# Kernel optimization log

Measured on AMD Instinct MI355X. Metric: run time of the kernel, lower is better.

Reference implementation:

```python
import jax, jax.numpy as jnp
import numpy as np

D = 64
N_NODES = 100000
N_EDGES = 1600000
N_GRAPHS = 64
IN_CH = 128
EDGE_DIM = 7
N_CONVS = 3  # layers after conv_first


def seg_softmax(logits, seg, n):
    m = jax.ops.segment_max(logits, seg, num_segments=n)
    e = jnp.exp(logits - m[seg])
    s = jax.ops.segment_sum(e, seg, num_segments=n)
    return e / (s[seg] + 1e-16)


def tconv(h, src, dst, edge_attr, Wq, bq, Wk, bk, Wv, bv, We, Ws, bs):
    # PyG TransformerConv, heads=1, concat=True, root_weight=True
    q = h @ Wq + bq          # [N, D]
    k = h @ Wk + bk
    v = h @ Wv + bv
    e = edge_attr @ We       # [E, D] (lin_edge has no bias)
    ke = k[src] + e          # key + edge per message
    alpha = jnp.sum(q[dst] * ke, axis=-1) / jnp.sqrt(jnp.float32(D))
    a = seg_softmax(alpha, dst, N_NODES)               # softmax over in-neighbors
    msg = a[:, None] * (v[src] + e)                    # [E, D]
    out = jax.ops.segment_sum(msg, dst, num_segments=N_NODES)
    return out + h @ Ws + bs                           # skip (lin_skip)


def setup_inputs() -> dict:
    key = jax.random.key(0)
    ks = iter(jax.random.split(key, 64))
    nrm = lambda shp, s=0.05: jax.random.normal(next(ks), shp, dtype=jnp.float32) * s
    inp = {}
    inp['x'] = jax.random.normal(next(ks), (N_NODES, IN_CH), dtype=jnp.float32)
    inp['edge_index'] = jax.random.randint(next(ks), (2, N_EDGES), 0, N_NODES, dtype=jnp.int32)
    inp['edge_attr'] = jax.random.normal(next(ks), (N_EDGES, EDGE_DIM), dtype=jnp.float32)
    inp['batch'] = jnp.sort(jax.random.randint(next(ks), (N_NODES,), 0, N_GRAPHS, dtype=jnp.int32))
    inp['y'] = jax.random.normal(next(ks), (N_GRAPHS, 6), dtype=jnp.float32)
    # conv_first (IN_CH -> D)
    inp['Wq0'] = nrm((IN_CH, D)); inp['bq0'] = jnp.zeros((D,), jnp.float32)
    inp['Wk0'] = nrm((IN_CH, D)); inp['bk0'] = jnp.zeros((D,), jnp.float32)
    inp['Wv0'] = nrm((IN_CH, D)); inp['bv0'] = jnp.zeros((D,), jnp.float32)
    inp['We0'] = nrm((EDGE_DIM, D))
    inp['Ws0'] = nrm((IN_CH, D)); inp['bs0'] = jnp.zeros((D,), jnp.float32)
    # stacked conv layers (D -> D), leading axis = layer
    inp['Wq'] = nrm((N_CONVS, D, D)); inp['bq'] = jnp.zeros((N_CONVS, D), jnp.float32)
    inp['Wk'] = nrm((N_CONVS, D, D)); inp['bk'] = jnp.zeros((N_CONVS, D), jnp.float32)
    inp['Wv'] = nrm((N_CONVS, D, D)); inp['bv'] = jnp.zeros((N_CONVS, D), jnp.float32)
    inp['We'] = nrm((N_CONVS, EDGE_DIM, D))
    inp['Ws'] = nrm((N_CONVS, D, D)); inp['bs'] = jnp.zeros((N_CONVS, D), jnp.float32)
    # gate_nn: Linear(D,D)+ReLU+Linear(D,1)
    inp['g1W'] = nrm((D, D)); inp['g1b'] = jnp.zeros((D,), jnp.float32)
    inp['g2W'] = nrm((D, 1)); inp['g2b'] = jnp.zeros((1,), jnp.float32)
    # 6 MLPs, each 64->32->16->8->1, stacked on leading expert axis
    inp['m0W'] = nrm((6, D, 32)); inp['m0b'] = jnp.zeros((6, 32), jnp.float32)
    inp['m1W'] = nrm((6, 32, 16)); inp['m1b'] = jnp.zeros((6, 16), jnp.float32)
    inp['m2W'] = nrm((6, 16, 8)); inp['m2b'] = jnp.zeros((6, 8), jnp.float32)
    inp['m3W'] = nrm((6, 8, 1)); inp['m3b'] = jnp.zeros((6, 1), jnp.float32)
    return inp


def reference(x, edge_attr, y, Wq0, bq0, Wk0, bk0, Wv0, bv0, We0, Ws0, bs0,
              Wq, bq, Wk, bk, Wv, bv, We, Ws, bs,
              g1W, g1b, g2W, g2b,
              m0W, m0b, m1W, m1b, m2W, m2b, m3W, m3b,
              edge_index, batch):
    src, dst = edge_index[0], edge_index[1]
    elu = jax.nn.elu
    outs = []
    h = elu(tconv(x, src, dst, edge_attr, Wq0, bq0, Wk0, bk0, Wv0, bv0, We0, Ws0, bs0))
    outs.append(h)
    for i in range(N_CONVS):
        h = tconv(h, src, dst, edge_attr, Wq[i], bq[i], Wk[i], bk[i],
                  Wv[i], bv[i], We[i], Ws[i], bs[i])
        if i != N_CONVS - 1:
            h = elu(h)
        outs.append(h)
    # JumpingKnowledge 'max'
    h = jnp.max(jnp.stack(outs, axis=0), axis=0)          # [N, D]
    # Global soft attention pooling
    gate = jax.nn.relu(h @ g1W + g1b) @ g2W + g2b         # [N, 1]
    gate = seg_softmax(gate[:, 0], batch, N_GRAPHS)[:, None]
    pooled = jax.ops.segment_sum(gate * h, batch, num_segments=N_GRAPHS)  # [G, D]
    # 6-way MLP ensemble (elu hidden)
    a = elu(jnp.einsum('gd,edh->egh', pooled, m0W) + m0b[:, None, :])
    a = elu(jnp.einsum('egh,ehk->egk', a, m1W) + m1b[:, None, :])
    a = elu(jnp.einsum('egk,ekj->egj', a, m2W) + m2b[:, None, :])
    preds = jnp.einsum('egj,ejo->ego', a, m3W) + m3b[:, None, :]  # [6, G, 1]
    preds = preds[:, :, 0].T                               # [G, 6]
    losses = jnp.sqrt(jnp.mean((preds - y) ** 2, axis=0))  # RMSE per target
    total_loss = jnp.sum(losses)
    return preds, total_loss
```

## Files before the change

### kernel.cpp

```cpp
#include <hip/hip_runtime.h>
#include <math.h>

#define N_NODES 100000
#define N_EDGES 1600000
#define N_GRAPHS 64
#define IN_CH 128
#define DIM 64
#define N_CONVS 3
#define NBLK 196
#define NPASS 8
#define PASS_SZ 12500

typedef const float* fp;
typedef unsigned int u32;
typedef unsigned short u16;
typedef __attribute__((ext_vector_type(8))) short short8v;
typedef __attribute__((ext_vector_type(4))) float f32x4;

__device__ inline u16 rne_bf16(float f) {
    u32 u = __float_as_uint(f);
    return (u16)((u + 0x7fffu + ((u >> 16) & 1u)) >> 16);
}
__device__ inline float bf16lo_f(u32 w) { return __uint_as_float(w << 16); }
__device__ inline float bf16hi_f(u32 w) { return __uint_as_float(w & 0xffff0000u); }

__global__ __launch_bounds__(256) void count_kernel(const int* __restrict__ dst, int* __restrict__ cnt) {
    int j = blockIdx.x * 256 + threadIdx.x;
    if (j < N_EDGES) {
        int d = dst[j];
        if ((unsigned)d < N_NODES) atomicAdd(&cnt[d], 1);
    }
}

__global__ __launch_bounds__(512) void scan1_kernel(const int* __restrict__ cnt, int* __restrict__ rp,
                                                    int* __restrict__ blksum) {
    __shared__ int tmp[512];
    int t = threadIdx.x, i = blockIdx.x * 512 + t;
    int v0 = (i < N_NODES) ? cnt[i] : 0;
    tmp[t] = v0;
    __syncthreads();
    for (int off = 1; off < 512; off <<= 1) {
        int add = (t >= off) ? tmp[t - off] : 0;
        __syncthreads();
        tmp[t] += add;
        __syncthreads();
    }
    if (i < N_NODES) rp[i] = tmp[t] - v0;
    if (t == 511) blksum[blockIdx.x] = tmp[511];
}

__global__ __launch_bounds__(256) void scan2_kernel(int* __restrict__ blksum) {
    __shared__ int tmp[256];
    int t = threadIdx.x;
    int v0 = (t < NBLK) ? blksum[t] : 0;
    tmp[t] = v0;
    __syncthreads();
    for (int off = 1; off < 256; off <<= 1) {
        int add = (t >= off) ? tmp[t - off] : 0;
        __syncthreads();
        tmp[t] += add;
        __syncthreads();
    }
    if (t < NBLK) blksum[t] = tmp[t] - v0;
}

__global__ __launch_bounds__(512) void scan3_kernel(int* __restrict__ rp, const int* __restrict__ blksum,
                                                    int* __restrict__ cursor) {
    int t = threadIdx.x, i = blockIdx.x * 512 + t;
    if (i < N_NODES) {
        int v = rp[i] + blksum[blockIdx.x];
        rp[i] = v;
        cursor[i] = v;
    }
    if (i == 0) rp[N_NODES] = N_EDGES;
}

__global__ __launch_bounds__(256) void cvt_ea_kernel(fp ea, uint4* __restrict__ eab_orig) {
    int j = blockIdx.x * 256 + threadIdx.x;
    if (j < N_EDGES) {
        size_t sb = (size_t)j * 7;
        u16 b[8];
#pragma unroll
        for (int c = 0; c < 7; ++c) b[c] = rne_bf16(ea[sb + c]);
        b[7] = 0;
        uint4 o;
        o.x = b[0] | ((u32)b[1] << 16);
        o.y = b[2] | ((u32)b[3] << 16);
        o.z = b[4] | ((u32)b[5] << 16);
        o.w = b[6] | ((u32)b[7] << 16);
        eab_orig[j] = o;
    }
}

__global__ __launch_bounds__(256) void scatter_pass_kernel(const int* __restrict__ src,
                                                           const int* __restrict__ dst,
                                                           const uint4* __restrict__ eab_orig,
                                                           int* __restrict__ cursor,
                                                           int* __restrict__ csr_src,
                                                           uint4* __restrict__ eab, int lo, int hi) {
    int j = blockIdx.x * 256 + threadIdx.x;
    if (j < N_EDGES) {
        int d = dst[j];
        if (d < lo || d >= hi || (unsigned)d >= N_NODES) return;
        int pos = atomicAdd(&cursor[d], 1);
        if ((unsigned)pos < N_EDGES) {
            int s = src[j];
            csr_src[pos] = ((unsigned)s < N_NODES) ? s : 0;
            eab[pos] = eab_orig[j];
        }
    }
}

__global__ __launch_bounds__(256) void cvt_bf16_kernel(const float* __restrict__ in, u16* __restrict__ out,
                                                       int n4) {
    int i = blockIdx.x * 256 + threadIdx.x;
    if (i < n4) {
        float4 v = reinterpret_cast<const float4*>(in)[i];
        ushort4 o;
        o.x = rne_bf16(v.x); o.y = rne_bf16(v.y); o.z = rne_bf16(v.z); o.w = rne_bf16(v.w);
        reinterpret_cast<ushort4*>(out)[i] = o;
    }
}

__global__ __launch_bounds__(256) void packW_kernel(fp Wq, fp Wk, fp Wv, fp Ws, u16* __restrict__ Bp,
                                                    int K) {
    int total = (K / 32) * 16 * 512;
    int tid = blockIdx.x * 256 + threadIdx.x;
    if (tid >= total) return;
    int j = tid & 7, l = (tid >> 3) & 63, fragid = tid >> 9;
    int tk = fragid >> 4, gtn = fragid & 15;
    int k = tk * 32 + ((l >> 4) << 3) + j;
    int n = (gtn << 4) + (l & 15);
    int mat = n >> 6, cn = n & 63;
    fp W = mat == 0 ? Wq : mat == 1 ? Wk : mat == 2 ? Wv : Ws;
    Bp[tid] = rne_bf16(W[k * 64 + cn]);
}

template <int K>
__global__ __launch_bounds__(256) void gemm_mfma_kernel(
    const u16* __restrict__ A, const u16* __restrict__ Bp,
    fp bq, fp bk, fp bv, fp bs,
    float* __restrict__ q, u16* __restrict__ kvp16, float* __restrict__ skb) {
    constexpr int NTK = K / 32;
    int wave = threadIdx.x >> 6;
    int l = threadIdx.x & 63;
    int lr = l & 15, lg = l >> 4;
    int row0 = blockIdx.x * 32;
    short8v a[2][NTK];
#pragma unroll
    for (int mi = 0; mi < 2; ++mi)
#pragma unroll
        for (int tk = 0; tk < NTK; ++tk)
            a[mi][tk] = *reinterpret_cast<const short8v*>(
                &A[(size_t)(row0 + mi * 16 + lr) * K + tk * 32 + lg * 8]);
    f32x4 c[2][4] = {};
#pragma unroll
    for (int tn = 0; tn < 4; ++tn) {
        int gtn = wave * 4 + tn;
#pragma unroll
        for (int tk = 0; tk < NTK; ++tk) {
            short8v b = *reinterpret_cast<const short8v*>(&Bp[((size_t)(tk * 16 + gtn) * 64 + l) * 8]);
            c[0][tn] = __builtin_amdgcn_mfma_f32_16x16x32_bf16(a[0][tk], b, c[0][tn], 0, 0, 0);
            c[1][tn] = __builtin_amdgcn_mfma_f32_16x16x32_bf16(a[1][tk], b, c[1][tn], 0, 0, 0);
        }
    }
    fp bias = wave == 0 ? bq : wave == 1 ? bk : wave == 2 ? bv : bs;
#pragma unroll
    for (int tn = 0; tn < 4; ++tn) {
        int cl = tn * 16 + lr;
        float bb = bias[cl];
#pragma unroll
        for (int mi = 0; mi < 2; ++mi)
#pragma unroll
            for (int r = 0; r < 4; ++r) {
                size_t row = row0 + mi * 16 + lg * 4 + r;
                float val = c[mi][tn][r] + bb;
                if (wave == 0) q[row * 64 + cl] = val * 0.125f;
                else if (wave == 3) skb[row * 64 + cl] = val;
                else if (wave == 1) kvp16[(row * 64 + cl) * 2] = rne_bf16(val);
                else kvp16[(row * 64 + cl) * 2 + 1] = rne_bf16(val);
            }
    }
}

__global__ __launch_bounds__(256) void node_kernel(
    const float* __restrict__ qs, const u32* __restrict__ kvp,
    const float* __restrict__ skb, const uint4* __restrict__ eab, fp We,
    const int* __restrict__ row_ptr, const int* __restrict__ csr_src,
    u16* __restrict__ hb, float* __restrict__ hmax, int act, int initmax) {
    int tid = threadIdx.x;
    int lane = tid & 63;
    int g = lane >> 4, fl = lane & 15;
    int gbase = g << 4;
    int n = blockIdx.x * 16 + (tid >> 6) * 4 + g;
    int f0 = fl * 4;
    float4 q4 = *reinterpret_cast<const float4*>(&qs[(size_t)n * 64 + f0]);
    float qw[7];
#pragma unroll
    for (int c = 0; c < 7; ++c) {
        float4 w4 = *reinterpret_cast<const float4*>(&We[c * 64 + f0]);
        float t = q4.x * w4.x + q4.y * w4.y + q4.z * w4.z + q4.w * w4.w;
        t += __shfl_xor(t, 1);
        t += __shfl_xor(t, 2);
        t += __shfl_xor(t, 4);
        t += __shfl_xor(t, 8);
        qw[c] = t;
    }
    int beg = row_ptr[n], end = row_ptr[n + 1];
    float s = 0.f;
    float ax = 0.f, ay = 0.f, az = 0.f, aw = 0.f;
    float r[7];
#pragma unroll
    for (int c = 0; c < 7; ++c) r[c] = 0.f;

    for (int p = beg; p < end; p += 4) {
        int svi = p + (fl & 3);
        svi = svi < end ? svi : end - 1;
        int sv = csr_src[svi];
#pragma unroll
        for (int j = 0; j < 4; ++j) {
            int pj = p + j;
            int pc = pj < end ? pj : end - 1;
            int sn = __shfl(sv, gbase + j);
            uint4 kv4 = *reinterpret_cast<const uint4*>(&kvp[(size_t)sn * 64 + f0]);
            uint4 e4 = eab[pc];
            float e0 = bf16lo_f(e4.x), e1 = bf16hi_f(e4.x);
            float e2 = bf16lo_f(e4.y), e3 = bf16hi_f(e4.y);
            float e4f = bf16lo_f(e4.z), e5 = bf16hi_f(e4.z);
            float e6 = bf16lo_f(e4.w);
            float al = qw[0] * e0 + qw[1] * e1 + qw[2] * e2 + qw[3] * e3 +
                       qw[4] * e4f + qw[5] * e5 + qw[6] * e6;
            float kf0 = bf16lo_f(kv4.x), vf0 = bf16hi_f(kv4.x);
            float kf1 = bf16lo_f(kv4.y), vf1 = bf16hi_f(kv4.y);
            float kf2 = bf16lo_f(kv4.z), vf2 = bf16hi_f(kv4.z);
            float kf3 = bf16lo_f(kv4.w), vf3 = bf16hi_f(kv4.w);
            float d = q4.x * kf0 + q4.y * kf1 + q4.z * kf2 + q4.w * kf3;
            d += __shfl_xor(d, 1);
            d += __shfl_xor(d, 2);
            d += __shfl_xor(d, 4);
            d += __shfl_xor(d, 8);
            float pe = (pj < end) ? __expf(al + d) : 0.f;
            s += pe;
            ax += pe * vf0; ay += pe * vf1; az += pe * vf2; aw += pe * vf3;
            r[0] += pe * e0; r[1] += pe * e1; r[2] += pe * e2; r[3] += pe * e3;
            r[4] += pe * e4f; r[5] += pe * e5; r[6] += pe * e6;
        }
    }
    float inv = 1.f / (s + 1e-16f);
    float o0 = ax, o1 = ay, o2 = az, o3 = aw;
#pragma unroll
    for (int c = 0; c < 7; ++c) {
        o0 += We[c * 64 + f0 + 0] * r[c];
        o1 += We[c * 64 + f0 + 1] * r[c];
        o2 += We[c * 64 + f0 + 2] * r[c];
        o3 += We[c * 64 + f0 + 3] * r[c];
    }
    float4 sk4 = *reinterpret_cast<const float4*>(&skb[(size_t)n * 64 + f0]);
    float4 res;
    res.x = o0 * inv + sk4.x;
    res.y = o1 * inv + sk4.y;
    res.z = o2 * inv + sk4.z;
    res.w = o3 * inv + sk4.w;
    if (act) {
        res.x = res.x > 0.f ? res.x : (__expf(res.x) - 1.f);
        res.y = res.y > 0.f ? res.y : (__expf(res.y) - 1.f);
        res.z = res.z > 0.f ? res.z : (__expf(res.z) - 1.f);
        res.w = res.w > 0.f ? res.w : (__expf(res.w) - 1.f);
    }
    ushort4 hb4;
    hb4.x = rne_bf16(res.x); hb4.y = rne_bf16(res.y); hb4.z = rne_bf16(res.z); hb4.w = rne_bf16(res.w);
    *reinterpret_cast<ushort4*>(&hb[(size_t)n * 64 + f0]) = hb4;
    if (initmax) {
        *reinterpret_cast<float4*>(&hmax[(size_t)n * 64 + f0]) = res;
    } else {
        float4 hm = *reinterpret_cast<const float4*>(&hmax[(size_t)n * 64 + f0]);
        hm.x = fmaxf(hm.x, res.x);
        hm.y = fmaxf(hm.y, res.y);
        hm.z = fmaxf(hm.z, res.z);
        hm.w = fmaxf(hm.w, res.w);
        *reinterpret_cast<float4*>(&hmax[(size_t)n * 64 + f0]) = hm;
    }
}

__global__ __launch_bounds__(256) void gate_kernel(const float* __restrict__ h, fp g1W, fp g1b, fp g2W,
                                                   fp g2b, float* __restrict__ gate) {
    __shared__ float hs[4][64];
    int w = threadIdx.x >> 6, lane = threadIdx.x & 63;
    int n = blockIdx.x * 4 + w;
    hs[w][lane] = h[(size_t)n * 64 + lane];
    __syncthreads();
    float a = 0.f;
    for (int f = 0; f < 64; ++f) a += hs[w][f] * g1W[f * 64 + lane];
    a = fmaxf(a + g1b[lane], 0.f);
    float val = a * g2W[lane];
#pragma unroll
    for (int off = 32; off; off >>= 1) val += __shfl_xor(val, off);
    if (lane == 0) gate[n] = val + g2b[0];
}

__global__ __launch_bounds__(256) void starts_kernel(const int* __restrict__ batch, int* __restrict__ starts) {
    int i = blockIdx.x * 256 + threadIdx.x;
    if (i >= N_NODES) return;
    if (i == 0) {
        int b = batch[0];
        for (int g = 0; g <= b && g <= N_GRAPHS; ++g) starts[g] = 0;
    } else {
        int b0 = batch[i - 1], b1 = batch[i];
        for (int g = b0 + 1; g <= b1 && g <= N_GRAPHS; ++g) starts[g] = i;
    }
    if (i == N_NODES - 1) {
        int b = batch[i];
        for (int g = b + 1; g <= N_GRAPHS; ++g) starts[g] = N_NODES;
    }
}

__global__ __launch_bounds__(256) void pool_kernel(const float* __restrict__ h, const float* __restrict__ gate,
                                                   const int* __restrict__ starts, float* __restrict__ pooled) {
    int g = blockIdx.x;
    int beg = starts[g], end = starts[g + 1];
    int tid = threadIdx.x, lane = tid & 63, w = tid >> 6;
    __shared__ float red[4];
    __shared__ float accs[4][64];
    float m = -INFINITY;
    for (int i = beg + tid; i < end; i += 256) m = fmaxf(m, gate[i]);
#pragma unroll
    for (int off = 32; off; off >>= 1) m = fmaxf(m, __shfl_xor(m, off));
    if (lane == 0) red[w] = m;
    __syncthreads();
    m = fmaxf(fmaxf(red[0], red[1]), fmaxf(red[2], red[3]));
    __syncthreads();
    float s = 0.f;
    for (int i = beg + tid; i < end; i += 256) s += __expf(gate[i] - m);
#pragma unroll
    for (int off = 32; off; off >>= 1) s += __shfl_xor(s, off);
    if (lane == 0) red[w] = s;
    __syncthreads();
    s = red[0] + red[1] + red[2] + red[3] + 1e-16f;
    float acc = 0.f;
    for (int i = beg + w; i < end; i += 4) {
        float p = __expf(gate[i] - m);
        acc += p * h[(size_t)i * 64 + lane];
    }
    accs[w][lane] = acc;
    __syncthreads();
    if (w == 0) pooled[g * 64 + lane] = (accs[0][lane] + accs[1][lane] + accs[2][lane] + accs[3][lane]) / s;
}

__global__ __launch_bounds__(256) void mlp_kernel(const float* __restrict__ pooled, fp m0W, fp m0b, fp m1W,
                                                  fp m1b, fp m2W, fp m2b, fp m3W, fp m3b,
                                                  float* __restrict__ out) {
    int e = blockIdx.x, tid = threadIdx.x;
    __shared__ float P[64 * 64];
    __shared__ float A1[64 * 32];
    __shared__ float A2[64 * 16];
    __shared__ float A3[64 * 8];
    for (int i = tid; i < 64 * 64; i += 256) P[i] = pooled[i];
    __syncthreads();
    fp W0 = m0W + e * 64 * 32; fp B0 = m0b + e * 32;
    for (int i = tid; i < 64 * 32; i += 256) {
        int g = i >> 5, c = i & 31;
        float a = B0[c];
        for (int f = 0; f < 64; ++f) a += P[g * 64 + f] * W0[f * 32 + c];
        A1[i] = a > 0.f ? a : (__expf(a) - 1.f);
    }
    __syncthreads();
    fp W1 = m1W + e * 32 * 16; fp B1 = m1b + e * 16;
    for (int i = tid; i < 64 * 16; i += 256) {
        int g = i >> 4, c = i & 15;
        float a = B1[c];
        for (int f = 0; f < 32; ++f) a += A1[g * 32 + f] * W1[f * 16 + c];
        A2[i] = a > 0.f ? a : (__expf(a) - 1.f);
    }
    __syncthreads();
    fp W2 = m2W + e * 16 * 8; fp B2 = m2b + e * 8;
    for (int i = tid; i < 64 * 8; i += 256) {
        int g = i >> 3, c = i & 7;
        float a = B2[c];
        for (int f = 0; f < 16; ++f) a += A2[g * 16 + f] * W2[f * 8 + c];
        A3[i] = a > 0.f ? a : (__expf(a) - 1.f);
    }
    __syncthreads();
    fp W3 = m3W + e * 8;
    if (tid < 64) {
        int g = tid;
        float a = m3b[e];
        for (int j = 0; j < 8; ++j) a += A3[g * 8 + j] * W3[j];
        out[g * 6 + e] = a;
    }
}

__global__ __launch_bounds__(64) void loss_kernel(const float* __restrict__ preds, fp y,
                                                  float* __restrict__ out) {
    int lane = threadIdx.x;
    float lsum = 0.f;
    if (lane < 6) {
        float acc = 0.f;
        for (int g = 0; g < 64; ++g) {
            float d = preds[g * 6 + lane] - y[g * 6 + lane];
            acc += d * d;
        }
        lsum = sqrtf(acc / 64.f);
    }
#pragma unroll
    for (int off = 32; off; off >>= 1) lsum += __shfl_xor(lsum, off);
    if (lane == 0) out[384] = lsum;
}

extern "C" void kernel_launch(void* const* d_in, const int* in_sizes, int n_in, void* d_out, int out_size,
                              void* d_ws, size_t ws_size, hipStream_t stream) {
    bool dictOrder = (in_sizes[1] == 2 * N_EDGES);
    int iEI = dictOrder ? 1 : 33;
    int iEA = dictOrder ? 2 : 1;
    int iBT = dictOrder ? 3 : 34;
    int iY  = dictOrder ? 4 : 2;
    int w0  = dictOrder ? 5 : 3;

    fp x = (fp)d_in[0];
    const int* ei = (const int*)d_in[iEI];
    fp eattr = (fp)d_in[iEA];
    const int* batch = (const int*)d_in[iBT];
    fp y = (fp)d_in[iY];
    fp Wq0 = (fp)d_in[w0 + 0], bq0 = (fp)d_in[w0 + 1], Wk0 = (fp)d_in[w0 + 2], bk0 = (fp)d_in[w0 + 3];
    fp Wv0 = (fp)d_in[w0 + 4], bv0 = (fp)d_in[w0 + 5], We0 = (fp)d_in[w0 + 6];
    fp Ws0 = (fp)d_in[w0 + 7], bs0 = (fp)d_in[w0 + 8];
    fp Wq = (fp)d_in[w0 + 9], bq = (fp)d_in[w0 + 10], Wk = (fp)d_in[w0 + 11], bk = (fp)d_in[w0 + 12];
    fp Wv = (fp)d_in[w0 + 13], bv = (fp)d_in[w0 + 14], Wel = (fp)d_in[w0 + 15];
    fp Ws = (fp)d_in[w0 + 16], bs = (fp)d_in[w0 + 17];
    fp g1W = (fp)d_in[w0 + 18], g1b = (fp)d_in[w0 + 19], g2W = (fp)d_in[w0 + 20], g2b = (fp)d_in[w0 + 21];
    fp m0W = (fp)d_in[w0 + 22], m0b = (fp)d_in[w0 + 23], m1W = (fp)d_in[w0 + 24], m1b = (fp)d_in[w0 + 25];
    fp m2W = (fp)d_in[w0 + 26], m2b = (fp)d_in[w0 + 27], m3W = (fp)d_in[w0 + 28], m3b = (fp)d_in[w0 + 29];

    const int* srcArr = ei;
    const int* dstArr = ei + N_EDGES;

    char* wsp = (char*)d_ws;
    auto alloc = [&](size_t bytes) -> void* {
        void* p = (void*)wsp;
        wsp += (bytes + 255) & ~(size_t)255;
        return p;
    };
    float* q = (float*)alloc((size_t)N_NODES * 64 * 4);
    u32* kvp = (u32*)alloc((size_t)N_NODES * 64 * 4);
    float* skb = (float*)alloc((size_t)N_NODES * 64 * 4);
    u16* hb = (u16*)alloc((size_t)N_NODES * 64 * 2);
    u16* xb = (u16*)alloc((size_t)N_NODES * IN_CH * 2);
    float* hmax = (float*)alloc((size_t)N_NODES * 64 * 4);
    float* gate = (float*)alloc((size_t)N_NODES * 4);
    float* pooled = (float*)alloc(64 * 64 * 4);
    int* row_ptr = (int*)alloc((N_NODES + 1) * 4);
    int* cursor = (int*)alloc((size_t)N_NODES * 4);
    int* csr_src = (int*)alloc((size_t)N_EDGES * 4);
    uint4* eab = (uint4*)alloc((size_t)N_EDGES * 16);
    uint4* eab_orig = (uint4*)alloc((size_t)N_EDGES * 16);
    u16* Bp0 = (u16*)alloc((size_t)(IN_CH / 32) * 16 * 512 * 2);
    u16* Bp1 = (u16*)alloc((size_t)(DIM / 32) * 16 * 512 * 2);
    u16* Bp2 = (u16*)alloc((size_t)(DIM / 32) * 16 * 512 * 2);
    u16* Bp3 = (u16*)alloc((size_t)(DIM / 32) * 16 * 512 * 2);
    int* blksum = (int*)alloc(256 * 4);
    int* starts = (int*)alloc((N_GRAPHS + 1) * 4);
    (void)ws_size;
    (void)n_in;

    float* outF = (float*)d_out;

    hipMemsetAsync(cursor, 0, (size_t)N_NODES * 4, stream);
    count_kernel<<<(N_EDGES + 255) / 256, 256, 0, stream>>>(dstArr, cursor);
    scan1_kernel<<<NBLK, 512, 0, stream>>>(cursor, row_ptr, blksum);
    scan2_kernel<<<1, 256, 0, stream>>>(blksum);
    scan3_kernel<<<NBLK, 512, 0, stream>>>(row_ptr, blksum, cursor);
    cvt_ea_kernel<<<(N_EDGES + 255) / 256, 256, 0, stream>>>(eattr, eab_orig);
    for (int p = 0; p < NPASS; ++p)
        scatter_pass_kernel<<<(N_EDGES + 255) / 256, 256, 0, stream>>>(
            srcArr, dstArr, eab_orig, cursor, csr_src, eab, p * PASS_SZ, (p + 1) * PASS_SZ);
    cvt_bf16_kernel<<<(N_NODES * IN_CH / 4 + 255) / 256, 256, 0, stream>>>(x, xb, N_NODES * IN_CH / 4);
    packW_kernel<<<((IN_CH / 32) * 16 * 512 + 255) / 256, 256, 0, stream>>>(Wq0, Wk0, Wv0, Ws0, Bp0, IN_CH);
    u16* Bps[3] = {Bp1, Bp2, Bp3};
    for (int i = 0; i < N_CONVS; ++i)
        packW_kernel<<<((DIM / 32) * 16 * 512 + 255) / 256, 256, 0, stream>>>(
            Wq + i * 4096, Wk + i * 4096, Wv + i * 4096, Ws + i * 4096, Bps[i], DIM);

    int nodeGrid = N_NODES / 16;
    gemm_mfma_kernel<IN_CH><<<N_NODES / 32, 256, 0, stream>>>(xb, Bp0, bq0, bk0, bv0, bs0, q, (u16*)kvp, skb);
    node_kernel<<<nodeGrid, 256, 0, stream>>>(q, kvp, skb, eab, We0, row_ptr, csr_src, hb, hmax, 1, 1);
    for (int i = 0; i < N_CONVS; ++i) {
        gemm_mfma_kernel<DIM><<<N_NODES / 32, 256, 0, stream>>>(hb, Bps[i], bq + i * 64, bk + i * 64,
                                                                bv + i * 64, bs + i * 64, q, (u16*)kvp, skb);
        node_kernel<<<nodeGrid, 256, 0, stream>>>(q, kvp, skb, eab, Wel + i * 448, row_ptr,
                                                  csr_src, hb, hmax, (i < N_CONVS - 1) ? 1 : 0, 0);
    }
    gate_kernel<<<N_NODES / 4, 256, 0, stream>>>(hmax, g1W, g1b, g2W, g2b, gate);
    starts_kernel<<<(N_NODES + 255) / 256, 256, 0, stream>>>(batch, starts);
    pool_kernel<<<N_GRAPHS, 256, 0, stream>>>(hmax, gate, starts, pooled);
    mlp_kernel<<<6, 256, 0, stream>>>(pooled, m0W, m0b, m1W, m1b, m2W, m2b, m3W, m3b, outF);
    loss_kernel<<<1, 64, 0, stream>>>(outF, y, outF);
}
```

Baseline: 898.2 us.

## Parallelize attention pooling across nodes with atomics instead of per-graph blocks

Replaces the 64-block per-graph pooling kernel (which serially scanned ~1560 nodes per graph) with node-parallel kernels. The gate kernel now computes the per-graph max through an order-preserving uint encoding and atomicMax. A separate kernel computes the exponentials and per-graph sums with wave-level reductions. A chunked accumulation kernel then atomically adds gate-weighted features into pooled, and normalization moves into the MLP kernel. The aim is to remove the low-occupancy tail of pool_kernel, at the cost of three extra memsets, float atomics with nondeterministic ordering, and an extra pass over the gate array.

```diff
diff --git a/kernel.cpp b/kernel.cpp
--- a/kernel.cpp
+++ b/kernel.cpp
@@ -23,6 +23,14 @@
 }
 __device__ inline float bf16lo_f(u32 w) { return __uint_as_float(w << 16); }
 __device__ inline float bf16hi_f(u32 w) { return __uint_as_float(w & 0xffff0000u); }
+__device__ inline u32 f_enc(float f) {
+    u32 u = __float_as_uint(f);
+    return (u & 0x80000000u) ? ~u : (u | 0x80000000u);
+}
+__device__ inline float f_dec(u32 e) {
+    u32 u = (e & 0x80000000u) ? (e & 0x7fffffffu) : ~e;
+    return __uint_as_float(u);
+}
 
 __global__ __launch_bounds__(256) void count_kernel(const int* __restrict__ dst, int* __restrict__ cnt) {
     int j = blockIdx.x * 256 + threadIdx.x;
@@ -283,7 +291,8 @@
 }
 
 __global__ __launch_bounds__(256) void gate_kernel(const float* __restrict__ h, fp g1W, fp g1b, fp g2W,
-                                                   fp g2b, float* __restrict__ gate) {
+                                                   fp g2b, const int* __restrict__ batch,
+                                                   float* __restrict__ gate, u32* __restrict__ gmaxEnc) {
     __shared__ float hs[4][64];
     int w = threadIdx.x >> 6, lane = threadIdx.x & 63;
     int n = blockIdx.x * 4 + w;
@@ -295,58 +304,62 @@
     float val = a * g2W[lane];
 #pragma unroll
     for (int off = 32; off; off >>= 1) val += __shfl_xor(val, off);
-    if (lane == 0) gate[n] = val + g2b[0];
-}
-
-__global__ __launch_bounds__(256) void starts_kernel(const int* __restrict__ batch, int* __restrict__ starts) {
+    if (lane == 0) {
+        float gv = val + g2b[0];
+        gate[n] = gv;
+        atomicMax(&gmaxEnc[batch[n]], f_enc(gv));
+    }
+}
+
+__global__ __launch_bounds__(256) void expsum_kernel(const int* __restrict__ batch,
+                                                     const u32* __restrict__ gmaxEnc,
+                                                     float* __restrict__ gate, float* __restrict__ gsum) {
     int i = blockIdx.x * 256 + threadIdx.x;
     if (i >= N_NODES) return;
-    if (i == 0) {
-        int b = batch[0];
-        for (int g = 0; g <= b && g <= N_GRAPHS; ++g) starts[g] = 0;
-    } else {
-        int b0 = batch[i - 1], b1 = batch[i];
-        for (int g = b0 + 1; g <= b1 && g <= N_GRAPHS; ++g) starts[g] = i;
-    }
-    if (i == N_NODES - 1) {
-        int b = batch[i];
-        for (int g = b + 1; g <= N_GRAPHS; ++g) starts[g] = N_NODES;
-    }
-}
-
-__global__ __launch_bounds__(256) void pool_kernel(const float* __restrict__ h, const float* __restrict__ gate,
-                                                   const int* __restrict__ starts, float* __restrict__ pooled) {
-    int g = blockIdx.x;
-    int beg = starts[g], end = starts[g + 1];
-    int tid = threadIdx.x, lane = tid & 63, w = tid >> 6;
-    __shared__ float red[4];
-    __shared__ float accs[4][64];
-    float m = -INFINITY;
-    for (int i = beg + tid; i < end; i += 256) m = fmaxf(m, gate[i]);
-#pragma unroll
-    for (int off = 32; off; off >>= 1) m = fmaxf(m, __shfl_xor(m, off));
-    if (lane == 0) red[w] = m;
-    __syncthreads();
-    m = fmaxf(fmaxf(red[0], red[1]), fmaxf(red[2], red[3]));
-    __syncthreads();
-    float s = 0.f;
-    for (int i = beg + tid; i < end; i += 256) s += __expf(gate[i] - m);
-#pragma unroll
-    for (int off = 32; off; off >>= 1) s += __shfl_xor(s, off);
-    if (lane == 0) red[w] = s;
-    __syncthreads();
-    s = red[0] + red[1] + red[2] + red[3] + 1e-16f;
+    int lane = threadIdx.x & 63;
+    int g = batch[i];
+    float p = __expf(gate[i] - f_dec(gmaxEnc[g]));
+    gate[i] = p;
+    int waveBase = i - lane;
+    bool fullWave = (waveBase + 63 < N_NODES);
+    if (fullWave) {
+        int g0 = __shfl(g, 0), g63 = __shfl(g, 63);
+        if (g0 == g63) {
+            float t = p;
+#pragma unroll
+            for (int off = 32; off; off >>= 1) t += __shfl_xor(t, off);
+            if (lane == 0) atomicAdd(&gsum[g], t);
+            return;
+        }
+    }
+    atomicAdd(&gsum[g], p);
+}
+
+#define PCHUNK 256
+__global__ __launch_bounds__(256) void pool_accum_kernel(const float* __restrict__ h,
+                                                         const float* __restrict__ gate,
+                                                         const int* __restrict__ batch,
+                                                         float* __restrict__ pooled) {
+    int w = threadIdx.x >> 6, lane = threadIdx.x & 63;
+    int base = blockIdx.x * PCHUNK;
     float acc = 0.f;
-    for (int i = beg + w; i < end; i += 4) {
-        float p = __expf(gate[i] - m);
-        acc += p * h[(size_t)i * 64 + lane];
-    }
-    accs[w][lane] = acc;
-    __syncthreads();
-    if (w == 0) pooled[g * 64 + lane] = (accs[0][lane] + accs[1][lane] + accs[2][lane] + accs[3][lane]) / s;
-}
-
-__global__ __launch_bounds__(256) void mlp_kernel(const float* __restrict__ pooled, fp m0W, fp m0b, fp m1W,
+    int cur = -1;
+    for (int t = 0; t < PCHUNK / 4; ++t) {
+        int i = base + w + 4 * t;
+        if (i >= N_NODES) break;
+        int g = batch[i];
+        if (g != cur) {
+            if (cur >= 0) atomicAdd(&pooled[cur * 64 + lane], acc);
+            acc = 0.f;
+            cur = g;
+        }
+        acc += gate[i] * h[(size_t)i * 64 + lane];
+    }
+    if (cur >= 0) atomicAdd(&pooled[cur * 64 + lane], acc);
+}
+
+__global__ __launch_bounds__(256) void mlp_kernel(const float* __restrict__ pooled,
+                                                  const float* __restrict__ gsum, fp m0W, fp m0b, fp m1W,
                                                   fp m1b, fp m2W, fp m2b, fp m3W, fp m3b,
                                                   float* __restrict__ out) {
     int e = blockIdx.x, tid = threadIdx.x;
@@ -354,7 +367,7 @@
     __shared__ float A1[64 * 32];
     __shared__ float A2[64 * 16];
     __shared__ float A3[64 * 8];
-    for (int i = tid; i < 64 * 64; i += 256) P[i] = pooled[i];
+    for (int i = tid; i < 64 * 64; i += 256) P[i] = pooled[i] / (gsum[i >> 6] + 1e-16f);
     __syncthreads();
     fp W0 = m0W + e * 64 * 32; fp B0 = m0b + e * 32;
     for (int i = tid; i < 64 * 32; i += 256) {
@@ -447,6 +460,8 @@
     float* hmax = (float*)alloc((size_t)N_NODES * 64 * 4);
     float* gate = (float*)alloc((size_t)N_NODES * 4);
     float* pooled = (float*)alloc(64 * 64 * 4);
+    u32* gmaxEnc = (u32*)alloc(N_GRAPHS * 4);
+    float* gsum = (float*)alloc(N_GRAPHS * 4);
     int* row_ptr = (int*)alloc((N_NODES + 1) * 4);
     int* cursor = (int*)alloc((size_t)N_NODES * 4);
     int* csr_src = (int*)alloc((size_t)N_EDGES * 4);
@@ -457,13 +472,15 @@
     u16* Bp2 = (u16*)alloc((size_t)(DIM / 32) * 16 * 512 * 2);
     u16* Bp3 = (u16*)alloc((size_t)(DIM / 32) * 16 * 512 * 2);
     int* blksum = (int*)alloc(256 * 4);
-    int* starts = (int*)alloc((N_GRAPHS + 1) * 4);
     (void)ws_size;
     (void)n_in;
 
     float* outF = (float*)d_out;
 
     hipMemsetAsync(cursor, 0, (size_t)N_NODES * 4, stream);
+    hipMemsetAsync(gmaxEnc, 0, N_GRAPHS * 4, stream);
+    hipMemsetAsync(gsum, 0, N_GRAPHS * 4, stream);
+    hipMemsetAsync(pooled, 0, 64 * 64 * 4, stream);
     count_kernel<<<(N_EDGES + 255) / 256, 256, 0, stream>>>(dstArr, cursor);
     scan1_kernel<<<NBLK, 512, 0, stream>>>(cursor, row_ptr, blksum);
     scan2_kernel<<<1, 256, 0, stream>>>(blksum);
@@ -488,9 +505,9 @@
         node_kernel<<<nodeGrid, 256, 0, stream>>>(q, kvp, skb, eab, Wel + i * 448, row_ptr,
                                                   csr_src, hb, hmax, (i < N_CONVS - 1) ? 1 : 0, 0);
     }
-    gate_kernel<<<N_NODES / 4, 256, 0, stream>>>(hmax, g1W, g1b, g2W, g2b, gate);
-    starts_kernel<<<(N_NODES + 255) / 256, 256, 0, stream>>>(batch, starts);
-    pool_kernel<<<N_GRAPHS, 256, 0, stream>>>(hmax, gate, starts, pooled);
-    mlp_kernel<<<6, 256, 0, stream>>>(pooled, m0W, m0b, m1W, m1b, m2W, m2b, m3W, m3b, outF);
+    gate_kernel<<<N_NODES / 4, 256, 0, stream>>>(hmax, g1W, g1b, g2W, g2b, batch, gate, gmaxEnc);
+    expsum_kernel<<<(N_NODES + 255) / 256, 256, 0, stream>>>(batch, gmaxEnc, gate, gsum);
+    pool_accum_kernel<<<(N_NODES + PCHUNK - 1) / PCHUNK, 256, 0, stream>>>(hmax, gate, batch, pooled);
+    mlp_kernel<<<6, 256, 0, stream>>>(pooled, gsum, m0W, m0b, m1W, m1b, m2W, m2b, m3W, m3b, outF);
     loss_kernel<<<1, 64, 0, stream>>>(outF, y, outF);
 }
```

New measurement: 1.573 ms. +75.1%, slower.
